# Optimization experiments

Hardware: AMD Instinct MI355X
Metric: run time of the kernel (lower is better)

## Reference

```python
import jax, jax.numpy as jnp
import numpy as np

VARIANCE = (0.1, 0.2)
THRESHOLD = 0.5
NEG_POS = 3


def point_form(boxes):
    # (cx,cy,w,h) -> (xmin,ymin,xmax,ymax)
    return jnp.concatenate([boxes[:, :2] - boxes[:, 2:] / 2,
                            boxes[:, :2] + boxes[:, 2:] / 2], axis=1)


def jaccard(a, b):
    # a: [T,4] xyxy truths, b: [P,4] xyxy priors -> IoU [T,P]
    lt = jnp.maximum(a[:, None, :2], b[None, :, :2])
    rb = jnp.minimum(a[:, None, 2:], b[None, :, 2:])
    wh = jnp.clip(rb - lt, 0.0)
    inter = wh[..., 0] * wh[..., 1]
    area_a = ((a[:, 2] - a[:, 0]) * (a[:, 3] - a[:, 1]))[:, None]
    area_b = ((b[:, 2] - b[:, 0]) * (b[:, 3] - b[:, 1]))[None, :]
    return inter / (area_a + area_b - inter)


def encode(matched, priors):
    g_cxcy = (matched[:, :2] + matched[:, 2:]) / 2 - priors[:, :2]
    g_cxcy = g_cxcy / (VARIANCE[0] * priors[:, 2:])
    g_wh = jnp.log((matched[:, 2:] - matched[:, :2]) / priors[:, 2:]) / VARIANCE[1]
    return jnp.concatenate([g_cxcy, g_wh], axis=1)


def match_one(truths, priors):
    # SSD match for one image; labels are zeroed in BiBoxLoss -> binary conf {0,1}
    overlaps = jaccard(truths, point_form(priors))          # [T,P]
    best_prior_idx = jnp.argmax(overlaps, axis=1)           # [T]
    best_truth_overlap = jnp.max(overlaps, axis=0)          # [P]
    best_truth_idx = jnp.argmax(overlaps, axis=0)           # [P]
    best_truth_overlap = best_truth_overlap.at[best_prior_idx].set(2.0)
    best_truth_idx = best_truth_idx.at[best_prior_idx].set(
        jnp.arange(truths.shape[0]))
    matched = truths[best_truth_idx]                        # [P,4]
    conf = jnp.where(best_truth_overlap < THRESHOLD, 0, 1)  # [P] int
    loc = encode(matched, priors)
    return loc, conf


def bibox_loss(loc_data, conf_data, priors, targets):
    num, num_priors = loc_data.shape[0], loc_data.shape[1]
    truths = targets[..., :4]                               # [B,T,4]
    loc_t, conf_t = jax.vmap(lambda t: match_one(t, priors))(truths)

    pos = conf_t > 0                                        # [B,P]
    # smooth L1 (sum) over positive priors
    ad = jnp.abs(loc_data - loc_t)
    sl1 = jnp.where(ad < 1.0, 0.5 * ad * ad, ad - 0.5)
    loss_l = jnp.sum(sl1 * pos[..., None].astype(loc_data.dtype))

    # per-prior CE (logsumexp - gathered logit) for hard-negative mining
    lse = jax.nn.logsumexp(conf_data, axis=-1)              # [B,P]
    gathered = jnp.take_along_axis(conf_data, conf_t[..., None], axis=-1)[..., 0]
    loss_c_all = lse - gathered                             # [B,P]

    loss_c_mine = jnp.where(pos, 0.0, loss_c_all)
    loss_idx = jnp.argsort(-loss_c_mine, axis=1)
    idx_rank = jnp.argsort(loss_idx, axis=1)                # rank of each prior
    num_pos = jnp.sum(pos.astype(jnp.int32), axis=1, keepdims=True)  # [B,1]
    num_neg = jnp.minimum(NEG_POS * num_pos, num_priors - 1)
    neg = idx_rank < num_neg                                # [B,P]

    sel = pos | neg
    loss_c = jnp.sum(jnp.where(sel, loss_c_all, 0.0))

    N = jnp.sum(num_pos).astype(loc_data.dtype)
    return loss_l / N, loss_c / N


def setup_inputs() -> dict:
    key = jax.random.key(0)
    k1, k2, k3, k4, k5, k6 = jax.random.split(key, 6)
    B, P, T = 32, 65536, 16
    loc_data = jax.random.normal(k1, (B, P, 4), dtype=jnp.float32)
    conf_data = jax.random.normal(k2, (B, P, 2), dtype=jnp.float32)
    # priors: valid center-form boxes
    pc = 0.15 + 0.7 * jax.random.uniform(k3, (P, 2), dtype=jnp.float32)
    pwh = 0.05 + 0.25 * jax.random.uniform(k4, (P, 2), dtype=jnp.float32)
    priors = jnp.concatenate([pc, pwh], axis=1)
    # targets: valid corner-form boxes + dummy label column (zeroed by the loss)
    tc = 0.2 + 0.6 * jax.random.uniform(k5, (B, T, 2), dtype=jnp.float32)
    twh = 0.05 + 0.25 * jax.random.uniform(k6, (B, T, 2), dtype=jnp.float32)
    boxes = jnp.concatenate([tc - twh / 2, tc + twh / 2], axis=-1)
    targets = jnp.concatenate(
        [boxes, jnp.ones((B, T, 1), dtype=jnp.float32)], axis=-1)
    return {"loc_data": loc_data, "conf_data": conf_data,
            "priors": priors, "targets": targets}


def reference(loc_data, conf_data, priors, targets):
    return bibox_loss(loc_data, conf_data, priors, targets)
```

## Files before the change

kernel.cpp:

```cpp
#include <hip/hip_runtime.h>

#define NB_ 32
#define NP_ 65536
#define NT_ 16
#define HB 1024
#define HSCALE 128.0f
#define NBX 64

__device__ __forceinline__ float softplus_(float x) {
    return fmaxf(x, 0.0f) + __logf(1.0f + __expf(-fabsf(x)));
}

__device__ __forceinline__ float iou_fast(float tx0, float ty0, float tx1, float ty1, float ta,
                                          float bx0, float by0, float bx1, float by1, float ar) {
    float lx = fmaxf(tx0, bx0), ly = fmaxf(ty0, by0);
    float rx = fminf(tx1, bx1), ry = fminf(ty1, by1);
    float w = fmaxf(rx - lx, 0.0f), h = fmaxf(ry - ly, 0.0f);
    float inter = w * h;
    return __fdividef(inter, ta + ar - inter);
}

#define DPP_STEP(x, t, ctrl, rmask, bmask, OP)                                          \
    t = __builtin_amdgcn_update_dpp(0, (x), (ctrl), (rmask), (bmask), true); OP;

__device__ __forceinline__ unsigned wave_max_u32(unsigned v) {
    int x = (int)v, t;
    DPP_STEP(x, t, 0x111, 0xf, 0xf, x = ((unsigned)t > (unsigned)x) ? t : x)
    DPP_STEP(x, t, 0x112, 0xf, 0xf, x = ((unsigned)t > (unsigned)x) ? t : x)
    DPP_STEP(x, t, 0x114, 0xf, 0xe, x = ((unsigned)t > (unsigned)x) ? t : x)
    DPP_STEP(x, t, 0x118, 0xf, 0xc, x = ((unsigned)t > (unsigned)x) ? t : x)
    DPP_STEP(x, t, 0x142, 0xa, 0xf, x = ((unsigned)t > (unsigned)x) ? t : x)
    DPP_STEP(x, t, 0x143, 0xc, 0xf, x = ((unsigned)t > (unsigned)x) ? t : x)
    return (unsigned)x;
}

__device__ __forceinline__ float wave_sum_f32(float v) {
    int x = __float_as_int(v), t;
    float f;
    DPP_STEP(x, t, 0x111, 0xf, 0xf, f = __int_as_float(x) + __int_as_float(t); x = __float_as_int(f))
    DPP_STEP(x, t, 0x112, 0xf, 0xf, f = __int_as_float(x) + __int_as_float(t); x = __float_as_int(f))
    DPP_STEP(x, t, 0x114, 0xf, 0xe, f = __int_as_float(x) + __int_as_float(t); x = __float_as_int(f))
    DPP_STEP(x, t, 0x118, 0xf, 0xc, f = __int_as_float(x) + __int_as_float(t); x = __float_as_int(f))
    DPP_STEP(x, t, 0x142, 0xa, 0xf, f = __int_as_float(x) + __int_as_float(t); x = __float_as_int(f))
    DPP_STEP(x, t, 0x143, 0xc, 0xf, f = __int_as_float(x) + __int_as_float(t); x = __float_as_int(f))
    return __int_as_float(x);
}

__device__ __forceinline__ int wave_sum_i32(int v) {
    int x = v, t;
    DPP_STEP(x, t, 0x111, 0xf, 0xf, x = x + t)
    DPP_STEP(x, t, 0x112, 0xf, 0xf, x = x + t)
    DPP_STEP(x, t, 0x114, 0xf, 0xe, x = x + t)
    DPP_STEP(x, t, 0x118, 0xf, 0xc, x = x + t)
    DPP_STEP(x, t, 0x142, 0xa, 0xf, x = x + t)
    DPP_STEP(x, t, 0x143, 0xc, 0xf, x = x + t)
    return x;
}

__global__ void __launch_bounds__(256) mainK(
    const float* __restrict__ loc, const float* __restrict__ conf,
    const float* __restrict__ priors, const float* __restrict__ targets,
    unsigned short* __restrict__ gcnt, float* __restrict__ gsum,
    unsigned long long* __restrict__ bestPart,
    float* __restrict__ part_ll, float* __restrict__ part_pc, int* __restrict__ part_np,
    unsigned* __restrict__ ticketB)
{
    const int bx = blockIdx.x, b = blockIdx.y, tid = threadIdx.x;

    __shared__ float4 trb[NT_];
    __shared__ float tra[NT_];
    __shared__ int hc[HB];
    __shared__ float hs[HB];
    __shared__ unsigned wkey[4][NT_], wp[4][NT_];
    __shared__ float sh_ll[4], sh_pc[4];
    __shared__ int sh_np[4];

    if (b == 0 && bx == 0 && tid < 33) ticketB[tid] = 0u;

    for (int i = tid; i < HB; i += 256) { hc[i] = 0; hs[i] = 0.0f; }
    if (tid < NT_) {
        const float* tp = targets + ((size_t)b * NT_ + tid) * 5;
        float x0 = tp[0], y0 = tp[1], x1 = tp[2], y1 = tp[3];
        trb[tid] = make_float4(x0, y0, x1, y1);
        tra[tid] = (x1 - x0) * (y1 - y0);
    }
    __syncthreads();

    const int pbase = bx * 1024 + tid;
    float pbx0[4], pby0[4], pbx1[4], pby1[4], par[4];
    float2 cxy[4];
#pragma unroll
    for (int i = 0; i < 4; i++) {
        float4 pr = ((const float4*)priors)[pbase + 256 * i];
        cxy[i] = ((const float2*)conf)[(size_t)b * NP_ + pbase + 256 * i];
        float hw = pr.z * 0.5f, hh = pr.w * 0.5f;
        pbx0[i] = pr.x - hw; pby0[i] = pr.y - hh;
        pbx1[i] = pr.x + hw; pby1[i] = pr.y + hh;
        par[i] = (pbx1[i] - pbx0[i]) * (pby1[i] - pby0[i]);
    }

    unsigned pkey[4] = {0u, 0u, 0u, 0u};
    unsigned tkey[NT_];
#pragma unroll
    for (int t = 0; t < NT_; t++) tkey[t] = 0u;

#pragma unroll
    for (int t = 0; t < NT_; t++) {
        float4 tb = trb[t];
        float ta = tra[t];
#pragma unroll
        for (int i = 0; i < 4; i++) {
            float iou = iou_fast(tb.x, tb.y, tb.z, tb.w, ta,
                                 pbx0[i], pby0[i], pbx1[i], pby1[i], par[i]);
            unsigned base = (__float_as_uint(iou) & 0xFFFFFFFCu) << 2;
            unsigned kt = base | (unsigned)(15 - t);
            unsigned kp = base | (unsigned)(15 - i);
            pkey[i] = (kt > pkey[i]) ? kt : pkey[i];
            tkey[t] = (kp > tkey[t]) ? kp : tkey[t];
        }
    }

    float ll_acc = 0.0f, pc_acc = 0.0f;
    int np_acc = 0;
#pragma unroll
    for (int i = 0; i < 4; i++) {
        int p = pbase + 256 * i;
        size_t bp = (size_t)b * NP_ + p;
        bool pos = (pkey[i] >= 0xFC000000u);
        float dd = cxy[i].y - cxy[i].x;
        float v = pos ? 0.0f : softplus_(dd);
        int bin = min(HB - 1, (int)(v * HSCALE));
        atomicAdd(&hc[bin], 1);
        atomicAdd(&hs[bin], v);
        if (pos) {
            np_acc++;
            pc_acc += softplus_(-dd);
            int t = 15 - (int)(pkey[i] & 15u);
            float4 tb = trb[t];
            float4 prv = ((const float4*)priors)[p];
            float gcx = ((tb.x + tb.z) * 0.5f - prv.x) / (0.1f * prv.z);
            float gcy = ((tb.y + tb.w) * 0.5f - prv.y) / (0.1f * prv.w);
            float gw = __logf((tb.z - tb.x) / prv.z) * 5.0f;
            float gh = __logf((tb.w - tb.y) / prv.w) * 5.0f;
            float4 ld = ((const float4*)loc)[bp];
            float d0 = fabsf(ld.x - gcx), d1 = fabsf(ld.y - gcy);
            float d2 = fabsf(ld.z - gw),  d3 = fabsf(ld.w - gh);
            ll_acc += (d0 < 1.0f) ? 0.5f * d0 * d0 : d0 - 0.5f;
            ll_acc += (d1 < 1.0f) ? 0.5f * d1 * d1 : d1 - 0.5f;
            ll_acc += (d2 < 1.0f) ? 0.5f * d2 * d2 : d2 - 0.5f;
            ll_acc += (d3 < 1.0f) ? 0.5f * d3 * d3 : d3 - 0.5f;
        }
    }

    const int wave = tid >> 6, lane = tid & 63;
#pragma unroll
    for (int t = 0; t < NT_; t++) {
        unsigned k = tkey[t];
        unsigned m = (unsigned)__builtin_amdgcn_readlane((int)wave_max_u32(k), 63);
        unsigned long long ball = __ballot(k == m);
        if (lane == 0) {
            int l = __ffsll((long long)ball) - 1;
            int ci = 15 - (int)(m & 15u);
            int p = bx * 1024 + ci * 256 + wave * 64 + l;
            wkey[wave][t] = m;
            wp[wave][t] = (unsigned)p;
        }
    }
    {
        float llw = wave_sum_f32(ll_acc);
        float pcw = wave_sum_f32(pc_acc);
        int npw = wave_sum_i32(np_acc);
        if (lane == 63) { sh_ll[wave] = llw; sh_pc[wave] = pcw; sh_np[wave] = npw; }
    }
    __syncthreads();

    if (tid < NT_) {
        unsigned bk = wkey[0][tid], bpv = wp[0][tid];
        for (int w = 1; w < 4; w++) {
            unsigned k2 = wkey[w][tid], p2 = wp[w][tid];
            if (k2 > bk || (k2 == bk && p2 < bpv)) { bk = k2; bpv = p2; }
        }
        unsigned long long pk = (((unsigned long long)bk) << 32) | (unsigned)(~bpv);
        bestPart[((size_t)b * NT_ + tid) * NBX + bx] = pk;
    }
    if (tid == 0) {
        part_ll[b * NBX + bx] = sh_ll[0] + sh_ll[1] + sh_ll[2] + sh_ll[3];
        part_pc[b * NBX + bx] = sh_pc[0] + sh_pc[1] + sh_pc[2] + sh_pc[3];
        part_np[b * NBX + bx] = sh_np[0] + sh_np[1] + sh_np[2] + sh_np[3];
    }
    unsigned short* gc = gcnt + ((size_t)(b * NBX + bx)) * HB;
    float* gs = gsum + ((size_t)(b * NBX + bx)) * HB;
    for (int i = tid; i < HB; i += 256) { gc[i] = (unsigned short)hc[i]; gs[i] = hs[i]; }
}

__global__ void __launch_bounds__(1024) finishK(
    const float* __restrict__ loc, const float* __restrict__ conf,
    const float* __restrict__ priors, const float* __restrict__ targets,
    const unsigned short* __restrict__ gcnt, const float* __restrict__ gsum,
    const unsigned long long* __restrict__ bestPart,
    const float* __restrict__ part_ll, const float* __restrict__ part_pc,
    const int* __restrict__ part_np,
    int* __restrict__ hcM, float* __restrict__ hsM,
    float* __restrict__ final_l, float* __restrict__ final_c, int* __restrict__ final_n,
    unsigned* __restrict__ ticketB, unsigned* __restrict__ ticket2,
    float* __restrict__ out)
{
    const int z = blockIdx.x, b = blockIdx.y, tid = threadIdx.x;
    __shared__ int hc[HB];
    __shared__ float hs[HB];
    __shared__ float4 trb[NT_];
    __shared__ float tra[NT_];
    __shared__ unsigned ps[NT_];
    __shared__ float s_dll, s_dpc, s_sll, s_spc;
    __shared__ int s_dnp, s_sn, s_last;
    __shared__ unsigned ccnt[16];
    __shared__ float csm[16];
    __shared__ unsigned s_old;

    if (tid < NT_) {
        const float* tp = targets + ((size_t)b * NT_ + tid) * 5;
        float x0 = tp[0], y0 = tp[1], x1 = tp[2], y1 = tp[3];
        trb[tid] = make_float4(x0, y0, x1, y1);
        tra[tid] = (x1 - x0) * (y1 - y0);
    }

    {
        const int binl = tid & 511;
        const int half = tid >> 9;
        const int bin  = z * 512 + binl;
        const size_t base = (size_t)(b * NBX) * HB + bin;
        const int j0 = half * 32;
        int c = 0; float s = 0.0f;
#pragma unroll 8
        for (int j = 0; j < 32; j++) {
            size_t o = base + (size_t)(j0 + j) * HB;
            c += (int)gcnt[o];
            s += gsum[o];
        }
        hc[half * 512 + binl] = c;
        hs[half * 512 + binl] = s;
    }
    __syncthreads();
    if (tid < 512) {
        int   mc = hc[tid] + hc[512 + tid];
        float ms = hs[tid] + hs[512 + tid];
        hcM[(size_t)b * HB + z * 512 + tid] = mc;
        hsM[(size_t)b * HB + z * 512 + tid] = ms;
    }
    __syncthreads();
    __threadfence();
    if (tid == 0) s_old = atomicAdd(&ticketB[b], 1u);
    __syncthreads();
    if (s_old != 1u) return;
    __threadfence();

    hc[tid] = hcM[(size_t)b * HB + tid];
    hs[tid] = hsM[(size_t)b * HB + tid];
    if (tid == 0) { s_dll = 0.0f; s_dpc = 0.0f; s_dnp = 0; s_last = 0; }

    {
        const int tr_i = tid >> 6, lane = tid & 63;
        unsigned long long v = bestPart[((size_t)b * NT_ + tr_i) * NBX + lane];
        for (int off = 32; off > 0; off >>= 1) {
            unsigned long long u = __shfl_down(v, off, 64);
            v = (u > v) ? u : v;
        }
        if (lane == 0) ps[tr_i] = ~((unsigned)(v & 0xffffffffULL));
    }
    if (tid < 64) {
        float lv = part_ll[b * NBX + tid];
        float pv = part_pc[b * NBX + tid];
        int nv = part_np[b * NBX + tid];
        lv = wave_sum_f32(lv); pv = wave_sum_f32(pv); nv = wave_sum_i32(nv);
        if (tid == 63) { s_sll = lv; s_spc = pv; s_sn = nv; }
    }
    __syncthreads();

    if (tid < NT_) {
        unsigned p = ps[tid];
        bool active = true;
        for (int u = tid + 1; u < NT_; u++)
            if (ps[u] == p) { active = false; break; }
        if (active) {
            float4 prv = ((const float4*)priors)[p];
            float hw = prv.z * 0.5f, hh = prv.w * 0.5f;
            float qx0 = prv.x - hw, qy0 = prv.y - hh;
            float qx1 = prv.x + hw, qy1 = prv.y + hh;
            float areab = (qx1 - qx0) * (qy1 - qy0);
            unsigned pk = 0u;
            for (int tt = 0; tt < NT_; tt++) {
                float4 tb = trb[tt];
                float iou = iou_fast(tb.x, tb.y, tb.z, tb.w, tra[tt],
                                     qx0, qy0, qx1, qy1, areab);
                unsigned cand = ((__float_as_uint(iou) & 0xFFFFFFFCu) << 2)
                              | (unsigned)(15 - tt);
                pk = (cand > pk) ? cand : pk;
            }
            bool pos0 = (pk >= 0xFC000000u);
            int t0 = 15 - (int)(pk & 15u);
            size_t bp = (size_t)b * NP_ + p;
            float2 cxyf = ((const float2*)conf)[bp];
            float dd = cxyf.y - cxyf.x;
            float4 ld = ((const float4*)loc)[bp];

            auto sl1_of = [&](int tt) -> float {
                float4 tb = trb[tt];
                float gcx = ((tb.x + tb.z) * 0.5f - prv.x) / (0.1f * prv.z);
                float gcy = ((tb.y + tb.w) * 0.5f - prv.y) / (0.1f * prv.w);
                float gw = __logf((tb.z - tb.x) / prv.z) * 5.0f;
                float gh = __logf((tb.w - tb.y) / prv.w) * 5.0f;
                float d0 = fabsf(ld.x - gcx), d1 = fabsf(ld.y - gcy);
                float d2 = fabsf(ld.z - gw),  d3 = fabsf(ld.w - gh);
                float s = (d0 < 1.0f) ? 0.5f * d0 * d0 : d0 - 0.5f;
                s += (d1 < 1.0f) ? 0.5f * d1 * d1 : d1 - 0.5f;
                s += (d2 < 1.0f) ? 0.5f * d2 * d2 : d2 - 0.5f;
                s += (d3 < 1.0f) ? 0.5f * d3 * d3 : d3 - 0.5f;
                return s;
            };
            float dll = sl1_of(tid) - (pos0 ? sl1_of(t0) : 0.0f);
            atomicAdd(&s_dll, dll);
            if (!pos0) {
                float v = softplus_(dd);
                int bin = min(HB - 1, (int)(v * HSCALE));
                atomicSub(&hc[bin], 1);
                atomicAdd(&hs[bin], -v);
                atomicAdd(&s_dpc, softplus_(-dd));
                atomicAdd(&s_dnp, 1);
            }
        }
    }
    __syncthreads();

    if (tid < 16) {
        unsigned cacc = 0; float sacc = 0.0f;
        for (int j = 0; j < 64; j++) { cacc += (unsigned)hc[tid * 64 + j]; sacc += hs[tid * 64 + j]; }
        ccnt[tid] = cacc; csm[tid] = sacc;
    }
    __syncthreads();

    if (tid == 0) {
        float sll = s_sll + s_dll;
        float spc = s_spc + s_dpc;
        int n = s_sn + s_dnp;
        int K = 3 * n;
        if (K > NP_ - 1) K = NP_ - 1;
        float tk = 0.0f;
        if (K > 0) {
            unsigned need = (unsigned)K, cum = 0;
            float s = 0.0f;
            int cb = 15;
            for (; cb > 0; --cb) {
                if (cum + ccnt[cb] >= need) break;
                cum += ccnt[cb]; s += csm[cb];
            }
            int bin = cb * 64 + 63;
            for (; bin > cb * 64; --bin) {
                if (cum + (unsigned)hc[bin] >= need) break;
                cum += (unsigned)hc[bin]; s += hs[bin];
            }
            unsigned rem = need - cum;
            int cv = hc[bin];
            float avg = (cv > 0) ? __fdividef(hs[bin], (float)cv) : 0.0f;
            tk = s + (float)rem * avg;
        }
        final_l[b] = sll;
        final_c[b] = spc + tk;
        final_n[b] = n;
        __threadfence();
        unsigned old = atomicAdd(ticket2, 1u);
        if (old == NB_ - 1) s_last = 1;
    }
    __syncthreads();

    if (s_last) {
        __threadfence();
        if (tid < 64) {
            float lv = 0.0f, cv = 0.0f;
            int nv = 0;
            if (tid < NB_) { lv = final_l[tid]; cv = final_c[tid]; nv = final_n[tid]; }
            for (int off = 32; off > 0; off >>= 1) {
                lv += __shfl_down(lv, off, 64);
                cv += __shfl_down(cv, off, 64);
                nv += __shfl_down(nv, off, 64);
            }
            if (tid == 0) {
                float fn = (float)nv;
                out[0] = lv / fn;
                out[1] = cv / fn;
            }
        }
    }
}

extern "C" void kernel_launch(void* const* d_in, const int* in_sizes, int n_in,
                              void* d_out, int out_size, void* d_ws, size_t ws_size,
                              hipStream_t stream) {
    const float* loc = (const float*)d_in[0];
    const float* conf = (const float*)d_in[1];
    const float* priors = (const float*)d_in[2];
    const float* targets = (const float*)d_in[3];
    float* out = (float*)d_out;

    char* w = (char*)d_ws;
    unsigned short* gcnt = (unsigned short*)w;
    float* gsum = (float*)(w + (4u << 20));
    char* acc = w + (12u << 20);
    unsigned long long* bestPart = (unsigned long long*)acc;
    float* part_ll = (float*)(acc + 262144);
    float* part_pc = (float*)(acc + 270336);
    int* part_np   = (int*)(acc + 278528);
    float* final_l = (float*)(acc + 286720);
    float* final_c = (float*)(acc + 286848);
    int* final_n   = (int*)(acc + 286976);
    unsigned* ticketB = (unsigned*)(acc + 287104);
    unsigned* ticket2 = ticketB + 32;
    int* hcM   = (int*)(acc + 287360);
    float* hsM = (float*)(acc + 287360 + 131072);

    mainK<<<dim3(NBX, NB_), 256, 0, stream>>>(loc, conf, priors, targets,
                                              gcnt, gsum, bestPart,
                                              part_ll, part_pc, part_np, ticketB);
    finishK<<<dim3(2, NB_), 1024, 0, stream>>>(loc, conf, priors, targets,
                                               gcnt, gsum, bestPart,
                                               part_ll, part_pc, part_np,
                                               hcM, hsM,
                                               final_l, final_c, final_n,
                                               ticketB, ticket2, out);
}
```

Baseline: 168.0 us.

## Replace atomic-ticket cross-block handoffs with per-image blocks and a final reduction kernel

The finish stage used two blocks per image that merged histograms through global memory and atomic tickets, plus a last-block ticket for the global reduction. Now one 1024-thread block per image reduces all 64 partial histograms directly, and a tiny third kernel does the final sum. This removes the global round trip, the fences and the ticket atomics. In exchange it halves finish-stage parallelism and adds one kernel launch.

```diff
diff --git a/kernel.cpp b/kernel.cpp
--- a/kernel.cpp
+++ b/kernel.cpp
@@ -62,8 +62,7 @@
     const float* __restrict__ priors, const float* __restrict__ targets,
     unsigned short* __restrict__ gcnt, float* __restrict__ gsum,
     unsigned long long* __restrict__ bestPart,
-    float* __restrict__ part_ll, float* __restrict__ part_pc, int* __restrict__ part_np,
-    unsigned* __restrict__ ticketB)
+    float* __restrict__ part_ll, float* __restrict__ part_pc, int* __restrict__ part_np)
 {
     const int bx = blockIdx.x, b = blockIdx.y, tid = threadIdx.x;
 
@@ -74,8 +73,6 @@
     __shared__ unsigned wkey[4][NT_], wp[4][NT_];
     __shared__ float sh_ll[4], sh_pc[4];
     __shared__ int sh_np[4];
-
-    if (b == 0 && bx == 0 && tid < 33) ticketB[tid] = 0u;
 
     for (int i = tid; i < HB; i += 256) { hc[i] = 0; hs[i] = 0.0f; }
     if (tid < NT_) {
@@ -200,23 +197,20 @@
     const unsigned long long* __restrict__ bestPart,
     const float* __restrict__ part_ll, const float* __restrict__ part_pc,
     const int* __restrict__ part_np,
-    int* __restrict__ hcM, float* __restrict__ hsM,
-    float* __restrict__ final_l, float* __restrict__ final_c, int* __restrict__ final_n,
-    unsigned* __restrict__ ticketB, unsigned* __restrict__ ticket2,
-    float* __restrict__ out)
+    float* __restrict__ final_l, float* __restrict__ final_c, int* __restrict__ final_n)
 {
-    const int z = blockIdx.x, b = blockIdx.y, tid = threadIdx.x;
+    const int b = blockIdx.x, tid = threadIdx.x;
     __shared__ int hc[HB];
     __shared__ float hs[HB];
     __shared__ float4 trb[NT_];
     __shared__ float tra[NT_];
     __shared__ unsigned ps[NT_];
     __shared__ float s_dll, s_dpc, s_sll, s_spc;
-    __shared__ int s_dnp, s_sn, s_last;
+    __shared__ int s_dnp, s_sn;
     __shared__ unsigned ccnt[16];
     __shared__ float csm[16];
-    __shared__ unsigned s_old;
-
+
+    if (tid == 0) { s_dll = 0.0f; s_dpc = 0.0f; s_dnp = 0; }
     if (tid < NT_) {
         const float* tp = targets + ((size_t)b * NT_ + tid) * 5;
         float x0 = tp[0], y0 = tp[1], x1 = tp[2], y1 = tp[3];
@@ -225,38 +219,18 @@
     }
 
     {
-        const int binl = tid & 511;
-        const int half = tid >> 9;
-        const int bin  = z * 512 + binl;
-        const size_t base = (size_t)(b * NBX) * HB + bin;
-        const int j0 = half * 32;
-        int c = 0; float s = 0.0f;
+        const size_t base = (size_t)(b * NBX) * HB + tid;
+        int cA = 0, cB = 0; float sA = 0.0f, sB = 0.0f;
 #pragma unroll 8
         for (int j = 0; j < 32; j++) {
-            size_t o = base + (size_t)(j0 + j) * HB;
-            c += (int)gcnt[o];
-            s += gsum[o];
-        }
-        hc[half * 512 + binl] = c;
-        hs[half * 512 + binl] = s;
-    }
-    __syncthreads();
-    if (tid < 512) {
-        int   mc = hc[tid] + hc[512 + tid];
-        float ms = hs[tid] + hs[512 + tid];
-        hcM[(size_t)b * HB + z * 512 + tid] = mc;
-        hsM[(size_t)b * HB + z * 512 + tid] = ms;
-    }
-    __syncthreads();
-    __threadfence();
-    if (tid == 0) s_old = atomicAdd(&ticketB[b], 1u);
-    __syncthreads();
-    if (s_old != 1u) return;
-    __threadfence();
-
-    hc[tid] = hcM[(size_t)b * HB + tid];
-    hs[tid] = hsM[(size_t)b * HB + tid];
-    if (tid == 0) { s_dll = 0.0f; s_dpc = 0.0f; s_dnp = 0; s_last = 0; }
+            size_t oA = base + (size_t)j * HB;
+            size_t oB = base + (size_t)(32 + j) * HB;
+            cA += (int)gcnt[oA]; sA += gsum[oA];
+            cB += (int)gcnt[oB]; sB += gsum[oB];
+        }
+        hc[tid] = cA + cB;
+        hs[tid] = sA + sB;
+    }
 
     {
         const int tr_i = tid >> 6, lane = tid & 63;
@@ -366,29 +340,26 @@
         final_l[b] = sll;
         final_c[b] = spc + tk;
         final_n[b] = n;
-        __threadfence();
-        unsigned old = atomicAdd(ticket2, 1u);
-        if (old == NB_ - 1) s_last = 1;
-    }
-    __syncthreads();
-
-    if (s_last) {
-        __threadfence();
-        if (tid < 64) {
-            float lv = 0.0f, cv = 0.0f;
-            int nv = 0;
-            if (tid < NB_) { lv = final_l[tid]; cv = final_c[tid]; nv = final_n[tid]; }
-            for (int off = 32; off > 0; off >>= 1) {
-                lv += __shfl_down(lv, off, 64);
-                cv += __shfl_down(cv, off, 64);
-                nv += __shfl_down(nv, off, 64);
-            }
-            if (tid == 0) {
-                float fn = (float)nv;
-                out[0] = lv / fn;
-                out[1] = cv / fn;
-            }
-        }
+    }
+}
+
+__global__ void __launch_bounds__(64) lastK(
+    const float* __restrict__ final_l, const float* __restrict__ final_c,
+    const int* __restrict__ final_n, float* __restrict__ out)
+{
+    const int tid = threadIdx.x;
+    float lv = 0.0f, cv = 0.0f;
+    int nv = 0;
+    if (tid < NB_) { lv = final_l[tid]; cv = final_c[tid]; nv = final_n[tid]; }
+    for (int off = 32; off > 0; off >>= 1) {
+        lv += __shfl_down(lv, off, 64);
+        cv += __shfl_down(cv, off, 64);
+        nv += __shfl_down(nv, off, 64);
+    }
+    if (tid == 0) {
+        float fn = (float)nv;
+        out[0] = lv / fn;
+        out[1] = cv / fn;
     }
 }
 
@@ -412,18 +383,13 @@
     float* final_l = (float*)(acc + 286720);
     float* final_c = (float*)(acc + 286848);
     int* final_n   = (int*)(acc + 286976);
-    unsigned* ticketB = (unsigned*)(acc + 287104);
-    unsigned* ticket2 = ticketB + 32;
-    int* hcM   = (int*)(acc + 287360);
-    float* hsM = (float*)(acc + 287360 + 131072);
 
     mainK<<<dim3(NBX, NB_), 256, 0, stream>>>(loc, conf, priors, targets,
                                               gcnt, gsum, bestPart,
-                                              part_ll, part_pc, part_np, ticketB);
-    finishK<<<dim3(2, NB_), 1024, 0, stream>>>(loc, conf, priors, targets,
-                                               gcnt, gsum, bestPart,
-                                               part_ll, part_pc, part_np,
-                                               hcM, hsM,
-                                               final_l, final_c, final_n,
-                                               ticketB, ticket2, out);
-}
+                                              part_ll, part_pc, part_np);
+    finishK<<<NB_, 1024, 0, stream>>>(loc, conf, priors, targets,
+                                      gcnt, gsum, bestPart,
+                                      part_ll, part_pc, part_np,
+                                      final_l, final_c, final_n);
+    lastK<<<1, 64, 0, stream>>>(final_l, final_c, final_n, out);
+}
```

After: 138.2 us. 17.8% less time.
